# Optimization experiments

Measured on AMD Instinct MI355X. Metric: run time of the kernel, lower is better.

## Reference

```python
import jax, jax.numpy as jnp
import numpy as np

DIM = 512
B, QL, KL = 8, 1024, 4096

def setup_inputs() -> dict:
    key = jax.random.key(0)
    k1, k2, k3 = jax.random.split(key, 3)
    output = jax.random.normal(k1, (B, QL, DIM), dtype=jnp.float32)
    context = jax.random.normal(k2, (B, KL, DIM), dtype=jnp.float32)
    # nn.Linear(2*dim, dim): weight [dim, 2*dim]; store transposed [2*dim, dim]
    W_out = jax.random.normal(k3, (DIM, 2 * DIM), dtype=jnp.float32) * (1.0 / np.sqrt(2 * DIM))
    b_out = jnp.zeros((DIM,), dtype=jnp.float32)
    return {"output": output, "context": context, "W_out": W_out, "b_out": b_out}

def reference(output, context, W_out, b_out):
    # scores: [B, QL, KL]
    attn = jnp.einsum("bqd,bkd->bqk", output, context)
    attn = jax.nn.softmax(attn, axis=-1)
    # mix: [B, QL, D]
    mix = jnp.einsum("bqk,bkd->bqd", attn, context)
    combined = jnp.concatenate([mix, output], axis=-1)  # [B, QL, 2D]
    out = jnp.tanh(jnp.einsum("bqe,de->bqd", combined, W_out) + b_out)
    return (out, attn)
```

## Files before the change

### kernel.cpp

```cpp
#include <hip/hip_runtime.h>
#include <math.h>

#define DIMM 512
#define NB 8
#define QLEN 1024
#define KLEN 4096

typedef __attribute__((ext_vector_type(4))) float floatx4;
typedef __attribute__((ext_vector_type(8))) short short8;
typedef __attribute__((ext_vector_type(4))) unsigned short ushort4v;
typedef __attribute__((ext_vector_type(8))) unsigned short ushort8v;

static __device__ __forceinline__ unsigned short f2bf(float f) {
    unsigned u = __builtin_bit_cast(unsigned, f);
    u += 0x7FFFu + ((u >> 16) & 1u);
    return (unsigned short)(u >> 16);
}
static __device__ __forceinline__ float bf2f(unsigned short h) {
    unsigned u = ((unsigned)h) << 16;
    return __builtin_bit_cast(float, u);
}
static __device__ __forceinline__ float fast_tanh(float x) {
    float e = __expf(-2.0f * fabsf(x));
    float t = (1.0f - e) / (1.0f + e);
    return copysignf(t, x);
}

static __device__ __forceinline__ void gload16(const unsigned short* g, unsigned short* l) {
    __builtin_amdgcn_global_load_lds(
        (__attribute__((address_space(1))) void*)const_cast<unsigned short*>(g),
        (__attribute__((address_space(3))) void*)l,
        16, 0, 0);
}

__global__ __launch_bounds__(256) void split_k(const float* __restrict__ x,
                                               unsigned short* __restrict__ dst) {
    int idx = blockIdx.x * 256 + threadIdx.x;
    float4 v = ((const float4*)x)[idx];
    int r = idx >> 7;
    int c = (idx & 127) << 2;
    float f[4] = {v.x, v.y, v.z, v.w};
    ushort4v hi, lo;
#pragma unroll
    for (int e = 0; e < 4; ++e) {
        unsigned short h = f2bf(f[e]);
        hi[e] = h;
        lo[e] = f2bf(f[e] - bf2f(h));
    }
    unsigned short* row = dst + ((size_t)r << 10);
    *(ushort4v*)(row + c) = lo;
    *(ushort4v*)(row + 512 + c) = hi;
}

__global__ __launch_bounds__(256) void conv_hi(const float* __restrict__ x,
                                               unsigned short* __restrict__ dst,
                                               int c4shift, int ldd, int off) {
    int idx = blockIdx.x * 256 + threadIdx.x;
    float4 v = ((const float4*)x)[idx];
    int r = idx >> c4shift;
    int c = (idx & ((1 << c4shift) - 1)) << 2;
    ushort4v hi;
    hi[0] = f2bf(v.x); hi[1] = f2bf(v.y); hi[2] = f2bf(v.z); hi[3] = f2bf(v.w);
    *(ushort4v*)(dst + (size_t)r * ldd + off + c) = hi;
}

__global__ __launch_bounds__(256) void prep_ctx(const float* __restrict__ ctx,
                                                unsigned short* __restrict__ hilo,
                                                unsigned short* __restrict__ ctxT) {
    __shared__ unsigned short tile[64][66];
    int b = blockIdx.z;
    int c0 = blockIdx.x * 64;
    int k0 = blockIdx.y * 64;
    const float* src = ctx + ((size_t)b * KLEN + k0) * DIMM + c0;
    unsigned short* hl = hilo + ((size_t)b * KLEN + k0) * 1024 + c0;
    int t = threadIdx.x;
    int rr = t >> 4, cc4 = (t & 15) * 4;
#pragma unroll
    for (int it = 0; it < 4; ++it) {
        int r = rr + it * 16;
        float4 v = *(const float4*)(src + (size_t)r * DIMM + cc4);
        float f[4] = {v.x, v.y, v.z, v.w};
        ushort4v hi, lo;
#pragma unroll
        for (int e = 0; e < 4; ++e) {
            unsigned short h = f2bf(f[e]);
            hi[e] = h;
            lo[e] = f2bf(f[e] - bf2f(h));
            tile[r][cc4 + e] = h;
        }
        *(ushort4v*)(hl + (size_t)r * 1024 + cc4) = hi;
        *(ushort4v*)(hl + (size_t)r * 1024 + 512 + cc4) = lo;
    }
    __syncthreads();
#pragma unroll
    for (int it = 0; it < 2; ++it) {
        int u = t + it * 256;
        int c = u >> 3;
        int kk = (u & 7) * 8;
        ushort8v o;
#pragma unroll
        for (int e = 0; e < 8; ++e) o[e] = tile[kk + e][c];
        *(ushort8v*)(ctxT + ((size_t)b * DIMM + c0 + c) * KLEN + k0 + kk) = o;
    }
}

__global__ __launch_bounds__(256) void softmax_k(float* __restrict__ S,
                                                 unsigned short* __restrict__ Pb) {
    size_t row = blockIdx.x;
    float* p = S + row * KLEN;
    int t = threadIdx.x;
    int lane = t & 63, wv = t >> 6;
    float4 v[4];
    float mx = -3.0e38f;
#pragma unroll
    for (int i = 0; i < 4; ++i) {
        v[i] = *(const float4*)(p + i * 1024 + t * 4);
        mx = fmaxf(mx, fmaxf(fmaxf(v[i].x, v[i].y), fmaxf(v[i].z, v[i].w)));
    }
#pragma unroll
    for (int m = 32; m >= 1; m >>= 1) mx = fmaxf(mx, __shfl_xor(mx, m, 64));
    __shared__ float redm[4], reds[4];
    if (lane == 0) redm[wv] = mx;
    __syncthreads();
    mx = fmaxf(fmaxf(redm[0], redm[1]), fmaxf(redm[2], redm[3]));
    float sum = 0.f;
#pragma unroll
    for (int i = 0; i < 4; ++i) {
        v[i].x = __expf(v[i].x - mx); v[i].y = __expf(v[i].y - mx);
        v[i].z = __expf(v[i].z - mx); v[i].w = __expf(v[i].w - mx);
        sum += v[i].x + v[i].y + v[i].z + v[i].w;
    }
#pragma unroll
    for (int m = 32; m >= 1; m >>= 1) sum += __shfl_xor(sum, m, 64);
    if (lane == 0) reds[wv] = sum;
    __syncthreads();
    float inv = 1.0f / (reds[0] + reds[1] + reds[2] + reds[3]);
    unsigned short* pb = Pb + row * KLEN;
#pragma unroll
    for (int i = 0; i < 4; ++i) {
        float4 w;
        w.x = v[i].x * inv; w.y = v[i].y * inv; w.z = v[i].z * inv; w.w = v[i].w * inv;
        *(float4*)(p + i * 1024 + t * 4) = w;
        ushort4v h;
        h[0] = f2bf(w.x); h[1] = f2bf(w.y); h[2] = f2bf(w.z); h[3] = f2bf(w.w);
        *(ushort4v*)(pb + i * 1024 + t * 4) = h;
    }
}

template <int EPI, bool REMAP, int BN, bool SWZ>
__global__ __launch_bounds__(256, 4) void gemm_bt(
    const unsigned short* __restrict__ A,
    const unsigned short* __restrict__ Bm,
    float* __restrict__ Cf, unsigned short* __restrict__ Cb,
    const float* __restrict__ bias,
    int Ktiles, long lda, long ldb, long ldc,
    long a_bs, long b_bs, long c_bs) {
    constexpr int NF = BN / 32;
    __shared__ unsigned short sA[128 * 64];
    __shared__ unsigned short sB[BN * 64];

    int bx, by, bz;
    if constexpr (SWZ) {
        int nx = gridDim.x, ny = gridDim.y;
        int nblk = nx * ny * (int)gridDim.z;
        int id = (int)blockIdx.x + nx * ((int)blockIdx.y + ny * (int)blockIdx.z);
        int wid = (id & 7) * (nblk >> 3) + (id >> 3);
        bx = wid % nx;
        int rem = wid / nx;
        by = rem % ny;
        bz = rem / ny;
    } else {
        bx = blockIdx.x; by = blockIdx.y; bz = blockIdx.z;
    }

    const int tid = threadIdx.x;
    const int lane = tid & 63;
    const int wv = tid >> 6;
    const int wm = wv >> 1, wn = wv & 1;
    const int mlane = lane & 15, quad = lane >> 4;
    const unsigned short* Ab = A + (size_t)bz * a_bs + (size_t)by * 128 * lda;
    const unsigned short* Bb = Bm + (size_t)bz * b_bs + (size_t)bx * BN * ldb;
    const int r8 = tid >> 3;
    const int c8 = (tid & 7) << 3;
    const int cg = ((tid & 7) ^ ((tid >> 3) & 7)) << 3;
    unsigned short* la = sA + r8 * 64 + c8;
    unsigned short* lb = sB + r8 * 64 + c8;

    floatx4 acc[4][NF] = {};

    for (int kt = 0; kt < Ktiles; ++kt) {
        long kv = (long)kt * 64;
        long ka = kv, kb = kv;
        if (REMAP) {
            ka = kv < 512 ? kv + 512 : (kv < 1024 ? kv : kv - 1024);
            kb = kv < 1024 ? kv : kv - 1024;
        }
        if (kt) __syncthreads();
        const unsigned short* ga = Ab + (size_t)r8 * lda + ka + cg;
        const unsigned short* gb = Bb + (size_t)r8 * ldb + kb + cg;
#pragma unroll
        for (int it = 0; it < 4; ++it)
            gload16(ga + (size_t)(it * 32) * lda, la + it * 2048);
#pragma unroll
        for (int it = 0; it < BN / 32; ++it)
            gload16(gb + (size_t)(it * 32) * ldb, lb + it * 2048);
        __syncthreads();
#pragma unroll
        for (int s = 0; s < 2; ++s) {
            const int swz = (((s * 4 + quad) ^ (mlane & 7)) << 3);
            short8 af[4];
#pragma unroll
            for (int i = 0; i < 4; ++i)
                af[i] = *(const short8*)(sA + (wm * 64 + i * 16 + mlane) * 64 + swz);
#pragma unroll
            for (int j = 0; j < NF; ++j) {
                short8 bfj = *(const short8*)(sB + (wn * (BN / 2) + j * 16 + mlane) * 64 + swz);
#pragma unroll
                for (int i = 0; i < 4; ++i)
                    acc[i][j] = __builtin_amdgcn_mfma_f32_16x16x32_bf16(af[i], bfj, acc[i][j], 0, 0, 0);
            }
        }
    }

    size_t crow0 = (size_t)by * 128 + wm * 64 + quad * 4;
    size_t ccol0 = (size_t)bx * BN + wn * (BN / 2) + mlane;
    size_t cbase = (size_t)bz * c_bs;
#pragma unroll
    for (int i = 0; i < 4; ++i) {
#pragma unroll
        for (int j = 0; j < NF; ++j) {
            size_t gr = crow0 + i * 16;
            size_t gc = ccol0 + j * 16;
#pragma unroll
            for (int r = 0; r < 4; ++r) {
                float vv = acc[i][j][r];
                size_t off = cbase + (gr + r) * ldc + gc;
                if (EPI == 0) Cf[off] = vv;
                else if (EPI == 1) Cb[off] = f2bf(vv);
                else Cf[off] = fast_tanh(vv + bias[gc]);
            }
        }
    }
}

extern "C" void kernel_launch(void* const* d_in, const int* in_sizes, int n_in,
                              void* d_out, int out_size, void* d_ws, size_t ws_size,
                              hipStream_t stream) {
    (void)in_sizes; (void)n_in; (void)out_size; (void)ws_size;
    const float* outp = (const float*)d_in[0];
    const float* ctx  = (const float*)d_in[1];
    const float* W    = (const float*)d_in[2];
    const float* bias = (const float*)d_in[3];

    float* out0 = (float*)d_out;
    float* attn = out0 + (size_t)NB * QLEN * DIMM;

    unsigned char* w = (unsigned char*)d_ws;
    unsigned short* R1 = (unsigned short*)(w);
    unsigned short* R2 = (unsigned short*)(w + (16ull << 20));
    unsigned short* R3 = (unsigned short*)(w + (80ull << 20));
    unsigned short* R4 = (unsigned short*)(w + (112ull << 20));

    split_k<<<4096, 256, 0, stream>>>(outp, R1);
    prep_ctx<<<dim3(8, 64, 8), 256, 0, stream>>>(ctx, R2, R3);
    conv_hi<<<512, 256, 0, stream>>>(W, R4, 8, 1024, 0);

    gemm_bt<0, true, 128, false><<<dim3(32, 8, 8), 256, 0, stream>>>(
        R1, R2, attn, nullptr, nullptr,
        24, 1024, 1024, 4096,
        (long)QLEN * 1024, (long)KLEN * 1024, (long)QLEN * KLEN);

    softmax_k<<<8192, 256, 0, stream>>>(attn, R2);

    gemm_bt<1, false, 64, true><<<dim3(8, 8, 8), 256, 0, stream>>>(
        R2, R3, nullptr, R1, nullptr,
        64, 4096, 4096, 1024,
        (long)QLEN * KLEN, (long)DIMM * KLEN, (long)QLEN * 1024);

    gemm_bt<2, false, 64, true><<<dim3(8, 64, 1), 256, 0, stream>>>(
        R1, R4, out0, nullptr, bias,
        16, 1024, 1024, 512, 0, 0, 0);
}
```

Baseline: 463.7 us.

## Replace QK^T GEMM with 256x256-tile 8-phase pipelined MFMA kernel

Adds a dedicated QK score kernel using 512-thread blocks with 256x256 output tiles, double-buffered LDS for A and B halves, and an interleaved schedule. Each K step is split into eight phases that alternate LDS fragment reads, global prefetch issue, and MFMA bursts, coordinated with explicit barriers, waitcnt and setprio. The goal is to raise arithmetic intensity and hide global and LDS latency behind MFMA work. In exchange it uses a large LDS footprint (128KB), which limits occupancy, and hand-tuned waitcnt logic that is fragile. The split-precision K remapping (kaOf/kbOf) is kept to match the previous 24-tile reduction.

```diff
diff --git a/kernel.cpp b/kernel.cpp
--- a/kernel.cpp
+++ b/kernel.cpp
@@ -145,6 +145,183 @@
         h[0] = f2bf(w.x); h[1] = f2bf(w.y); h[2] = f2bf(w.z); h[3] = f2bf(w.w);
         *(ushort4v*)(pb + i * 1024 + t * 4) = h;
     }
+}
+
+__global__ __launch_bounds__(512, 2) void qk_8ph(
+    const unsigned short* __restrict__ Aq,
+    const unsigned short* __restrict__ Bc,
+    float* __restrict__ Cf) {
+    __shared__ unsigned short sA[2][2][8192];
+    __shared__ unsigned short sB[2][2][8192];
+    const int tid = threadIdx.x;
+    const int lane = tid & 63;
+    const int wv = tid >> 6;
+    const int wm = wv >> 2;
+    const int wn = wv & 3;
+    const int wb = wn >> 1;
+    const int mlane = lane & 15, quad = lane >> 4;
+    const unsigned short* Ab = Aq + (size_t)blockIdx.z * (QLEN * 1024) + (size_t)blockIdx.y * 256 * 1024;
+    const unsigned short* Bb = Bc + (size_t)blockIdx.z * ((size_t)KLEN * 1024) + (size_t)blockIdx.x * 256 * 1024;
+    const int cg = ((tid & 7) ^ ((tid >> 3) & 7)) << 3;
+    const int srow = tid >> 3;
+
+    auto kaOf = [](int t) -> long { long kv = t * 64L; return kv < 512 ? kv + 512 : (kv < 1024 ? kv : kv - 1024); };
+    auto kbOf = [](int t) -> long { long kv = t * 64L; return kv < 1024 ? kv : kv - 1024; };
+    auto stage = [&](const unsigned short* gbase, unsigned short* lbase, long kofs) {
+        const unsigned short* g = gbase + (size_t)srow * 1024 + kofs + cg;
+        gload16(g, lbase);
+        gload16(g + (size_t)64 * 1024, lbase + 4096);
+    };
+    auto stA = [&](int q, int h, int t) { stage(Ab + (size_t)h * 128 * 1024, &sA[q][h][0] + tid * 8, kaOf(t)); };
+    auto stB = [&](int q, int h, int t) { stage(Bb + (size_t)h * 128 * 1024, &sB[q][h][0] + tid * 8, kbOf(t)); };
+
+    const unsigned short* const pA[2] = {&sA[0][wm][0], &sA[1][wm][0]};
+    const unsigned short* const pB[2] = {&sB[0][wb][0] + (wn & 1) * 4096,
+                                         &sB[1][wb][0] + (wn & 1) * 4096};
+    auto rdA = [&](int q, int m, int s) -> short8 {
+        return *(const short8*)(pA[q] + (m * 16 + mlane) * 64 + (((s * 4 + quad) ^ (mlane & 7)) << 3));
+    };
+    auto rdB = [&](int q, int n, int s) -> short8 {
+        return *(const short8*)(pB[q] + (n * 16 + mlane) * 64 + (((s * 4 + quad) ^ (mlane & 7)) << 3));
+    };
+
+#define QK_BAR1() __builtin_amdgcn_s_barrier();                          \
+    asm volatile("s_waitcnt lgkmcnt(0)" ::: "memory");                   \
+    __builtin_amdgcn_sched_barrier(0);                                   \
+    __builtin_amdgcn_s_setprio(1)
+#define QK_BAR2() __builtin_amdgcn_s_setprio(0);                         \
+    __builtin_amdgcn_s_barrier();                                        \
+    __builtin_amdgcn_sched_barrier(0)
+
+    floatx4 acc[8][4] = {};
+
+    stA(0, 0, 0); stA(0, 1, 0); stB(0, 0, 0); stB(0, 1, 0);
+    stA(1, 0, 1); stA(1, 1, 1);
+    asm volatile("s_waitcnt vmcnt(4)" ::: "memory");
+    __builtin_amdgcn_s_barrier();
+    __builtin_amdgcn_sched_barrier(0);
+
+    for (int i = 0; i < 12; ++i) {
+        const int u = 2 * i, v = u + 1;
+        const bool sg = (i < 11);
+        short8 afL[8], afH[8], bfA[4], bfB[4];
+#pragma unroll
+        for (int m = 0; m < 4; ++m) { afL[m * 2] = rdA(0, m, 0); afL[m * 2 + 1] = rdA(0, m, 1); }
+#pragma unroll
+        for (int n = 0; n < 2; ++n) { bfA[n * 2] = rdB(0, n, 0); bfA[n * 2 + 1] = rdB(0, n, 1); }
+        stB(1, 0, v);
+        QK_BAR1();
+#pragma unroll
+        for (int m = 0; m < 4; ++m)
+#pragma unroll
+            for (int n = 0; n < 2; ++n)
+#pragma unroll
+                for (int s = 0; s < 2; ++s)
+                    acc[m][n] = __builtin_amdgcn_mfma_f32_16x16x32_bf16(afL[m * 2 + s], bfA[n * 2 + s], acc[m][n], 0, 0, 0);
+        QK_BAR2();
+#pragma unroll
+        for (int m = 0; m < 4; ++m) { afH[m * 2] = rdA(0, m + 4, 0); afH[m * 2 + 1] = rdA(0, m + 4, 1); }
+        stB(1, 1, v);
+        QK_BAR1();
+#pragma unroll
+        for (int m = 0; m < 4; ++m)
+#pragma unroll
+            for (int n = 0; n < 2; ++n)
+#pragma unroll
+                for (int s = 0; s < 2; ++s)
+                    acc[m + 4][n] = __builtin_amdgcn_mfma_f32_16x16x32_bf16(afH[m * 2 + s], bfA[n * 2 + s], acc[m + 4][n], 0, 0, 0);
+        QK_BAR2();
+#pragma unroll
+        for (int n = 0; n < 2; ++n) { bfB[n * 2] = rdB(0, n + 2, 0); bfB[n * 2 + 1] = rdB(0, n + 2, 1); }
+        if (sg) stA(0, 0, u + 2);
+        QK_BAR1();
+#pragma unroll
+        for (int m = 0; m < 4; ++m)
+#pragma unroll
+            for (int n = 0; n < 2; ++n)
+#pragma unroll
+                for (int s = 0; s < 2; ++s)
+                    acc[m][n + 2] = __builtin_amdgcn_mfma_f32_16x16x32_bf16(afL[m * 2 + s], bfB[n * 2 + s], acc[m][n + 2], 0, 0, 0);
+        QK_BAR2();
+        if (sg) stA(0, 1, u + 2);
+        QK_BAR1();
+#pragma unroll
+        for (int m = 0; m < 4; ++m)
+#pragma unroll
+            for (int n = 0; n < 2; ++n)
+#pragma unroll
+                for (int s = 0; s < 2; ++s)
+                    acc[m + 4][n + 2] = __builtin_amdgcn_mfma_f32_16x16x32_bf16(afH[m * 2 + s], bfB[n * 2 + s], acc[m + 4][n + 2], 0, 0, 0);
+        __builtin_amdgcn_s_setprio(0);
+        if (sg) { asm volatile("s_waitcnt vmcnt(4)" ::: "memory"); }
+        else    { asm volatile("s_waitcnt vmcnt(0)" ::: "memory"); }
+        __builtin_amdgcn_s_barrier();
+        __builtin_amdgcn_sched_barrier(0);
+#pragma unroll
+        for (int m = 0; m < 4; ++m) { afL[m * 2] = rdA(1, m, 0); afL[m * 2 + 1] = rdA(1, m, 1); }
+#pragma unroll
+        for (int n = 0; n < 2; ++n) { bfA[n * 2] = rdB(1, n, 0); bfA[n * 2 + 1] = rdB(1, n, 1); }
+        if (sg) stB(0, 0, u + 2);
+        QK_BAR1();
+#pragma unroll
+        for (int m = 0; m < 4; ++m)
+#pragma unroll
+            for (int n = 0; n < 2; ++n)
+#pragma unroll
+                for (int s = 0; s < 2; ++s)
+                    acc[m][n] = __builtin_amdgcn_mfma_f32_16x16x32_bf16(afL[m * 2 + s], bfA[n * 2 + s], acc[m][n], 0, 0, 0);
+        QK_BAR2();
+#pragma unroll
+        for (int m = 0; m < 4; ++m) { afH[m * 2] = rdA(1, m + 4, 0); afH[m * 2 + 1] = rdA(1, m + 4, 1); }
+        if (sg) stB(0, 1, u + 2);
+        QK_BAR1();
+#pragma unroll
+        for (int m = 0; m < 4; ++m)
+#pragma unroll
+            for (int n = 0; n < 2; ++n)
+#pragma unroll
+                for (int s = 0; s < 2; ++s)
+                    acc[m + 4][n] = __builtin_amdgcn_mfma_f32_16x16x32_bf16(afH[m * 2 + s], bfA[n * 2 + s], acc[m + 4][n], 0, 0, 0);
+        QK_BAR2();
+#pragma unroll
+        for (int n = 0; n < 2; ++n) { bfB[n * 2] = rdB(1, n + 2, 0); bfB[n * 2 + 1] = rdB(1, n + 2, 1); }
+        if (sg) stA(1, 0, v + 2);
+        QK_BAR1();
+#pragma unroll
+        for (int m = 0; m < 4; ++m)
+#pragma unroll
+            for (int n = 0; n < 2; ++n)
+#pragma unroll
+                for (int s = 0; s < 2; ++s)
+                    acc[m][n + 2] = __builtin_amdgcn_mfma_f32_16x16x32_bf16(afL[m * 2 + s], bfB[n * 2 + s], acc[m][n + 2], 0, 0, 0);
+        QK_BAR2();
+        if (sg) stA(1, 1, v + 2);
+        QK_BAR1();
+#pragma unroll
+        for (int m = 0; m < 4; ++m)
+#pragma unroll
+            for (int n = 0; n < 2; ++n)
+#pragma unroll
+                for (int s = 0; s < 2; ++s)
+                    acc[m + 4][n + 2] = __builtin_amdgcn_mfma_f32_16x16x32_bf16(afH[m * 2 + s], bfB[n * 2 + s], acc[m + 4][n + 2], 0, 0, 0);
+        __builtin_amdgcn_s_setprio(0);
+        if (sg) { asm volatile("s_waitcnt vmcnt(4)" ::: "memory"); }
+        __builtin_amdgcn_s_barrier();
+        __builtin_amdgcn_sched_barrier(0);
+    }
+#undef QK_BAR1
+#undef QK_BAR2
+
+    const size_t crow0 = (size_t)blockIdx.y * 256 + wm * 128 + quad * 4;
+    const size_t ccol0 = (size_t)blockIdx.x * 256 + wn * 64 + mlane;
+    float* Cb = Cf + (size_t)blockIdx.z * ((size_t)QLEN * KLEN);
+#pragma unroll
+    for (int m = 0; m < 8; ++m)
+#pragma unroll
+        for (int n = 0; n < 4; ++n)
+#pragma unroll
+            for (int r = 0; r < 4; ++r)
+                Cb[(crow0 + m * 16 + r) * KLEN + ccol0 + n * 16] = acc[m][n][r];
 }
 
 template <int EPI, bool REMAP, int BN, bool SWZ>
@@ -265,10 +442,7 @@
     prep_ctx<<<dim3(8, 64, 8), 256, 0, stream>>>(ctx, R2, R3);
     conv_hi<<<512, 256, 0, stream>>>(W, R4, 8, 1024, 0);
 
-    gemm_bt<0, true, 128, false><<<dim3(32, 8, 8), 256, 0, stream>>>(
-        R1, R2, attn, nullptr, nullptr,
-        24, 1024, 1024, 4096,
-        (long)QLEN * 1024, (long)KLEN * 1024, (long)QLEN * KLEN);
+    qk_8ph<<<dim3(16, 4, 8), 512, 0, stream>>>(R1, R2, attn);
 
     softmax_k<<<8192, 256, 0, stream>>>(attn, R2);
 
```

Result: no change. 459.5 us (-0.9%).
